# Kernel tuning notes

Measured on AMD Instinct MI355X. Metric: run time of the kernel, lower is better.

Reference implementation:

```python
import jax, jax.numpy as jnp
import numpy as np

N = 50000      # nodes
E = 800000     # edges
H = 4          # attention heads
C = 64         # per-head channels (channel_in = channel_out = 64)
DIN = 128      # raw node feature dim (lazy Linear infers this)
D1 = H * C     # 256 = channel_in*4 concat dim
EPS = 1e-16    # PyG softmax eps
LN_EPS = 1e-5


def setup_inputs() -> dict:
    key = jax.random.key(0)
    ks = jax.random.split(key, 20)
    p = lambda k, shape: jax.random.normal(k, shape, jnp.float32) * 0.05
    return {
        "x": jax.random.normal(ks[0], (N, DIN), jnp.float32),
        "edge_index": jax.random.randint(ks[1], (2, E), 0, N, jnp.int32),
        # conv1 (GATConv with separate src/dst transforms, bipartite lazy mode)
        "Wsrc1": p(ks[2], (DIN, D1)), "Wdst1": p(ks[3], (DIN, D1)),
        "atts1": p(ks[4], (H, C)), "attd1": p(ks[5], (H, C)), "b1": p(ks[6], (D1,)),
        # lin1 skip
        "Wlin1": p(ks[7], (DIN, D1)), "blin1": p(ks[8], (D1,)),
        # LayerNorm
        "gamma": jnp.ones((D1,), jnp.float32), "beta": jnp.zeros((D1,), jnp.float32),
        # conv2
        "Wsrc2": p(ks[9], (D1, D1)), "Wdst2": p(ks[10], (D1, D1)),
        "atts2": p(ks[11], (H, C)), "attd2": p(ks[12], (H, C)), "b2": p(ks[13], (D1,)),
        # lin2 skip
        "Wlin2": p(ks[14], (D1, D1)), "blin2": p(ks[15], (D1,)),
    }


def gat_conv(x, src, dst, Wsrc, Wdst, atts, attd, bias):
    """PyG GATConv: gather -> leaky_relu score -> segment softmax over dst -> scatter-add."""
    n = x.shape[0]
    xs = (x @ Wsrc).reshape(n, H, C)   # source-side transform
    xd = (x @ Wdst).reshape(n, H, C)   # destination-side transform
    a_s = jnp.sum(xs * atts, axis=-1)  # [N,H]
    a_d = jnp.sum(xd * attd, axis=-1)  # [N,H]
    e = jax.nn.leaky_relu(a_s[src] + a_d[dst], 0.2)          # [E,H]
    m = jax.ops.segment_max(e, dst, num_segments=n)           # [N,H]
    m = jnp.where(jnp.isfinite(m), m, 0.0)                    # nodes with no in-edges
    ex = jnp.exp(e - m[dst])
    den = jax.ops.segment_sum(ex, dst, num_segments=n)
    alpha = ex / (den[dst] + EPS)                             # [E,H]
    out = jax.ops.segment_sum(xs[src] * alpha[:, :, None], dst, num_segments=n)
    return out.reshape(n, H * C) + bias                       # concat heads + bias


def reference(x, edge_index, Wsrc1, Wdst1, atts1, attd1, b1, Wlin1, blin1,
              gamma, beta, Wsrc2, Wdst2, atts2, attd2, b2, Wlin2, blin2):
    src, dst = edge_index[0], edge_index[1]
    h = gat_conv(x, src, dst, Wsrc1, Wdst1, atts1, attd1, b1) + x @ Wlin1 + blin1
    mu = jnp.mean(h, axis=-1, keepdims=True)
    var = jnp.mean((h - mu) ** 2, axis=-1, keepdims=True)
    h = (h - mu) * jax.lax.rsqrt(var + LN_EPS) * gamma + beta
    h = jax.nn.relu(h)
    out = gat_conv(h, src, dst, Wsrc2, Wdst2, atts2, attd2, b2) + h @ Wlin2 + blin2
    return out
```

## Files before the change

### kernel.cpp

```cpp
#include <hip/hip_runtime.h>
#include <float.h>

constexpr int DIN = 128;
constexpr int D1  = 256;
constexpr int HH  = 4;
constexpr int CC  = 64;

typedef _Float16 f16;
typedef __attribute__((ext_vector_type(2))) _Float16 f16x2;
typedef __attribute__((ext_vector_type(4))) _Float16 f16x4;
typedef __attribute__((ext_vector_type(8))) _Float16 f16x8;
typedef __attribute__((ext_vector_type(4))) float f32x4;

#if __has_builtin(__builtin_amdgcn_fdot2)
#define HAS_FDOT2 1
#else
#define HAS_FDOT2 0
#endif

__device__ __forceinline__ float wave_sum(float v) {
    #pragma unroll
    for (int off = 32; off > 0; off >>= 1) v += __shfl_down(v, off, 64);
    return v;
}

__global__ __launch_bounds__(256) void cvt_f16_kernel(
        const float* __restrict__ in, f16* __restrict__ out, int n4) {
    int i = blockIdx.x * 256 + threadIdx.x;
    if (i >= n4) return;
    float4 v = reinterpret_cast<const float4*>(in)[i];
    f16x4 o = {(f16)v.x, (f16)v.y, (f16)v.z, (f16)v.w};
    reinterpret_cast<f16x4*>(out)[i] = o;
}

__global__ __launch_bounds__(256) void pack_w_kernel(
        const float* __restrict__ Wa, const float* __restrict__ Wb,
        f16* __restrict__ Wpa, f16* __restrict__ Wpb, int K) {
    int idx = blockIdx.x * 256 + threadIdx.x;
    if (idx >= K * 256) return;
    int j    = idx & 7;
    int lane = (idx >> 3) & 63;
    int t    = idx >> 9;
    int ct   = t & 15, kt = t >> 4;
    int k    = kt * 32 + (lane >> 4) * 8 + j;
    int col  = ct * 16 + (lane & 15);
    size_t widx = (size_t)k * D1 + col;
    Wpa[idx] = (f16)Wa[widx];
    Wpb[idx] = (f16)Wb[widx];
}

__global__ __launch_bounds__(512) void make_v_kernel(
        const float* __restrict__ Wsrc, const float* __restrict__ Wdst,
        const float* __restrict__ atts, const float* __restrict__ attd,
        float* __restrict__ Vs, float* __restrict__ Vd) {
    int k = blockIdx.x;
    int w = threadIdx.x >> 6, lane = threadIdx.x & 63;
    int mat = w >> 2, h = w & 3;
    const float* W   = mat ? Wdst : Wsrc;
    const float* att = mat ? attd : atts;
    float v = W[(size_t)k * D1 + h * CC + lane] * att[h * CC + lane];
    v = wave_sum(v);
    if (lane == 0) (mat ? Vd : Vs)[k * HH + h] = v;
}

template <int K>
__global__ __launch_bounds__(256) void scores_kernel(
        const f16* __restrict__ X, const float* __restrict__ Vs,
        const float* __restrict__ Vd, float* __restrict__ a_s,
        float* __restrict__ a_d, int n) {
    constexpr int C  = K / 4;
    constexpr int SH = (C == 64) ? 6 : 5;
    __shared__ float4 VsL[K + 4];
    __shared__ float4 VdL[K + 4];
    for (int k = threadIdx.x; k < K; k += 256) {
        int ki = k + (k >> SH);
        VsL[ki] = reinterpret_cast<const float4*>(Vs)[k];
        VdL[ki] = reinterpret_cast<const float4*>(Vd)[k];
    }
    __syncthreads();

    const int lane  = threadIdx.x & 63;
    const int wid   = threadIdx.x >> 6;
    const int node  = blockIdx.x * 64 + wid * 16 + (lane >> 2);
    const int chunk = lane & 3;
    const int nodec = min(node, n - 1);
    const f16* xp = X + (size_t)nodec * K + chunk * C;

    f16x8 xv[C / 8];
    #pragma unroll
    for (int b = 0; b < C / 8; ++b)
        xv[b] = reinterpret_cast<const f16x8*>(xp)[b];

    float ps0 = 0.f, ps1 = 0.f, ps2 = 0.f, ps3 = 0.f;
    float pd0 = 0.f, pd1 = 0.f, pd2 = 0.f, pd3 = 0.f;
    #pragma unroll
    for (int b = 0; b < C / 8; ++b) {
        #pragma unroll
        for (int t = 0; t < 8; ++t) {
            int k  = chunk * C + b * 8 + t;
            int ki = k + (k >> SH);
            float xf = (float)xv[b][t];
            float4 vs = VsL[ki];
            float4 vd = VdL[ki];
            ps0 = fmaf(xf, vs.x, ps0); ps1 = fmaf(xf, vs.y, ps1);
            ps2 = fmaf(xf, vs.z, ps2); ps3 = fmaf(xf, vs.w, ps3);
            pd0 = fmaf(xf, vd.x, pd0); pd1 = fmaf(xf, vd.y, pd1);
            pd2 = fmaf(xf, vd.z, pd2); pd3 = fmaf(xf, vd.w, pd3);
        }
    }
    #pragma unroll
    for (int off = 1; off <= 2; off <<= 1) {
        ps0 += __shfl_xor(ps0, off, 64); ps1 += __shfl_xor(ps1, off, 64);
        ps2 += __shfl_xor(ps2, off, 64); ps3 += __shfl_xor(ps3, off, 64);
        pd0 += __shfl_xor(pd0, off, 64); pd1 += __shfl_xor(pd1, off, 64);
        pd2 += __shfl_xor(pd2, off, 64); pd3 += __shfl_xor(pd3, off, 64);
    }
    if (node < n) {
        float psv = chunk == 0 ? ps0 : chunk == 1 ? ps1 : chunk == 2 ? ps2 : ps3;
        float pdv = chunk == 0 ? pd0 : chunk == 1 ? pd1 : chunk == 2 ? pd2 : pd3;
        a_s[node * 4 + chunk] = psv;
        a_d[node * 4 + chunk] = pdv;
    }
}

__global__ __launch_bounds__(256) void zero_int_kernel(int* __restrict__ p, int n) {
    int i = blockIdx.x * 256 + threadIdx.x;
    if (i < n) p[i] = 0;
}

__global__ __launch_bounds__(256) void deg_kernel(
        const int* __restrict__ dst, int* __restrict__ deg, int ne) {
    int e = blockIdx.x * 256 + threadIdx.x;
    if (e < ne) atomicAdd(deg + dst[e], 1);
}

__global__ __launch_bounds__(1024) void scan_phase1(
        const int* __restrict__ deg, int* __restrict__ partial,
        int* __restrict__ blocksum, int n) {
    __shared__ int tmp[1024];
    const int tid = threadIdx.x;
    int i = blockIdx.x * 1024 + tid;
    int v = (i < n) ? deg[i] : 0;
    tmp[tid] = v;
    __syncthreads();
    #pragma unroll
    for (int off = 1; off < 1024; off <<= 1) {
        int t = (tid >= off) ? tmp[tid - off] : 0;
        __syncthreads();
        tmp[tid] += t;
        __syncthreads();
    }
    if (i < n) partial[i] = tmp[tid];
    if (tid == 1023) blocksum[blockIdx.x] = tmp[1023];
}

__global__ __launch_bounds__(64) void scan_phase2(int* __restrict__ bs, int nb) {
    int lane = threadIdx.x;
    if (nb <= 64) {
        int v = (lane < nb) ? bs[lane] : 0;
        #pragma unroll
        for (int off = 1; off < 64; off <<= 1) {
            int t = __shfl_up(v, off, 64);
            if (lane >= off) v += t;
        }
        if (lane < nb) bs[lane] = v;
    } else if (lane == 0) {
        int acc = 0;
        for (int i = 0; i < nb; ++i) { acc += bs[i]; bs[i] = acc; }
    }
}

__global__ __launch_bounds__(1024) void scan_phase3(
        const int* __restrict__ partial, const int* __restrict__ bs,
        const int* __restrict__ deg, int* __restrict__ rowptr,
        int* __restrict__ degcur, int n) {
    int i = blockIdx.x * 1024 + threadIdx.x;
    if (i >= n) return;
    int add  = blockIdx.x ? bs[blockIdx.x - 1] : 0;
    int incl = partial[i] + add;
    rowptr[i + 1] = incl;
    degcur[i] = incl - deg[i];
    if (i == 0) rowptr[0] = 0;
}

__global__ __launch_bounds__(256) void fill_kernel(
        const int* __restrict__ src, const int* __restrict__ dst,
        int* __restrict__ cursor, int* __restrict__ srcs_csr, int ne) {
    int e = blockIdx.x * 256 + threadIdx.x;
    if (e >= ne) return;
    int pos = atomicAdd(cursor + dst[e], 1);
    srcs_csr[pos] = src[e];
}

template <int K, typename TO2>
__global__ __launch_bounds__(256) void gemm_dual_mfma(
        const f16* __restrict__ A, const f16* __restrict__ Wp1,
        const f16* __restrict__ Wp2, const float* __restrict__ bias1,
        const float* __restrict__ bias2, f16* __restrict__ O1,
        TO2* __restrict__ O2, int n) {
    constexpr int KT = K / 32;
    const int lane = threadIdx.x & 63;
    const int w    = threadIdx.x >> 6;
    const int row0 = blockIdx.x * 64;
    const int col0 = w * 64;

    f32x4 acc1[4][4], acc2[4][4];
    const f32x4 zero = {0.f, 0.f, 0.f, 0.f};
    #pragma unroll
    for (int i = 0; i < 4; ++i)
        #pragma unroll
        for (int j = 0; j < 4; ++j) { acc1[i][j] = zero; acc2[i][j] = zero; }

    const f16* Arow[4];
    #pragma unroll
    for (int rf = 0; rf < 4; ++rf) {
        int ar = min(row0 + rf * 16 + (lane & 15), n - 1);
        Arow[rf] = A + (size_t)ar * K + (lane >> 4) * 8;
    }
    const f16* Wb1 = Wp1 + ((size_t)(w * 4) * 64 + lane) * 8;
    const f16* Wb2 = Wp2 + ((size_t)(w * 4) * 64 + lane) * 8;

    #pragma unroll
    for (int kt = 0; kt < KT; ++kt) {
        f16x8 a[4];
        #pragma unroll
        for (int rf = 0; rf < 4; ++rf)
            a[rf] = *reinterpret_cast<const f16x8*>(Arow[rf] + kt * 32);
        #pragma unroll
        for (int cf = 0; cf < 4; ++cf) {
            f16x8 b1v = *reinterpret_cast<const f16x8*>(Wb1 + (size_t)(kt * 16 + cf) * 512);
            f16x8 b2v = *reinterpret_cast<const f16x8*>(Wb2 + (size_t)(kt * 16 + cf) * 512);
            #pragma unroll
            for (int rf = 0; rf < 4; ++rf) {
                acc1[rf][cf] = __builtin_amdgcn_mfma_f32_16x16x32_f16(a[rf], b1v, acc1[rf][cf], 0, 0, 0);
                acc2[rf][cf] = __builtin_amdgcn_mfma_f32_16x16x32_f16(a[rf], b2v, acc2[rf][cf], 0, 0, 0);
            }
        }
    }

    #pragma unroll
    for (int cf = 0; cf < 4; ++cf) {
        const int col = col0 + cf * 16 + (lane & 15);
        const float bsum = bias1[col] + bias2[col];
        #pragma unroll
        for (int rf = 0; rf < 4; ++rf) {
            #pragma unroll
            for (int r = 0; r < 4; ++r) {
                const int row = row0 + rf * 16 + (lane >> 4) * 4 + r;
                if (row < n) {
                    O1[(size_t)row * D1 + col] = (f16)acc1[rf][cf][r];
                    O2[(size_t)row * D1 + col] = (TO2)(acc2[rf][cf][r] + bsum);
                }
            }
        }
    }
}

__device__ __forceinline__ float sel4(float4 v, int h) {
    return h == 0 ? v.x : h == 1 ? v.y : h == 2 ? v.z : v.w;
}
__device__ __forceinline__ float4 lrelu4(float4 as, float4 ad) {
    float4 e;
    e.x = as.x + ad.x; e.x = e.x > 0.f ? e.x : 0.2f * e.x;
    e.y = as.y + ad.y; e.y = e.y > 0.f ? e.y : 0.2f * e.y;
    e.z = as.z + ad.z; e.z = e.z > 0.f ? e.z : 0.2f * e.z;
    e.w = as.w + ad.w; e.w = e.w > 0.f ? e.w : 0.2f * e.w;
    return e;
}

#define ALDS_STRIDE 66

__device__ __forceinline__ float4 gat_node_acc(
        const int* __restrict__ srcs, const float* __restrict__ a_s,
        const f16* __restrict__ xs, f16* __restrict__ alds,
        float4 ad4, int base, int deg, int lane) {
    const int h  = lane >> 4;
    float4 den = {0.f, 0.f, 0.f, 0.f};
    float4 acc = {0.f, 0.f, 0.f, 0.f};
    const f16* arow = alds + h * ALDS_STRIDE;

    for (int c0 = 0; c0 < deg; c0 += 64) {
        const int cnt = min(64, deg - c0);
        const int idx = c0 + lane;
        const int sl  = srcs[base + min(idx, deg - 1)];
        {
            float4 as = *reinterpret_cast<const float4*>(a_s + (size_t)sl * 4);
            float4 e = lrelu4(as, ad4);
            const bool valid = idx < deg;
            float a0 = valid ? __expf(e.x) : 0.f;
            float a1 = valid ? __expf(e.y) : 0.f;
            float a2 = valid ? __expf(e.z) : 0.f;
            float a3 = valid ? __expf(e.w) : 0.f;
            den.x += a0; den.y += a1; den.z += a2; den.w += a3;
            alds[0 * ALDS_STRIDE + lane] = (f16)a0;
            alds[1 * ALDS_STRIDE + lane] = (f16)a1;
            alds[2 * ALDS_STRIDE + lane] = (f16)a2;
            alds[3 * ALDS_STRIDE + lane] = (f16)a3;
        }
        asm volatile("s_waitcnt lgkmcnt(0)" ::: "memory");

        const int sv = sl;
        for (int i = 0; i < cnt; i += 2) {
            int s1 = __shfl(sv, i, 64);
            int s2 = __shfl(sv, i + 1, 64);
            f16x2 al2 = *reinterpret_cast<const f16x2*>(arow + i);
            uint2 xA = *reinterpret_cast<const uint2*>(xs + (size_t)s1 * D1 + lane * 4);
            uint2 xB = *reinterpret_cast<const uint2*>(xs + (size_t)s2 * D1 + lane * 4);
#if HAS_FDOT2
            unsigned p0 = __builtin_amdgcn_perm(xA.x, xB.x, 0x01000504u);
            unsigned p1 = __builtin_amdgcn_perm(xA.x, xB.x, 0x03020706u);
            unsigned p2 = __builtin_amdgcn_perm(xA.y, xB.y, 0x01000504u);
            unsigned p3 = __builtin_amdgcn_perm(xA.y, xB.y, 0x03020706u);
            acc.x = __builtin_amdgcn_fdot2(__builtin_bit_cast(f16x2, p0), al2, acc.x, false);
            acc.y = __builtin_amdgcn_fdot2(__builtin_bit_cast(f16x2, p1), al2, acc.y, false);
            acc.z = __builtin_amdgcn_fdot2(__builtin_bit_cast(f16x2, p2), al2, acc.z, false);
            acc.w = __builtin_amdgcn_fdot2(__builtin_bit_cast(f16x2, p3), al2, acc.w, false);
#else
            f16x4 a4 = __builtin_bit_cast(f16x4, xA);
            f16x4 b4 = __builtin_bit_cast(f16x4, xB);
            float alA = (float)al2.x, alB = (float)al2.y;
            acc.x = fmaf((float)a4[0], alA, acc.x); acc.x = fmaf((float)b4[0], alB, acc.x);
            acc.y = fmaf((float)a4[1], alA, acc.y); acc.y = fmaf((float)b4[1], alB, acc.y);
            acc.z = fmaf((float)a4[2], alA, acc.z); acc.z = fmaf((float)b4[2], alB, acc.z);
            acc.w = fmaf((float)a4[3], alA, acc.w); acc.w = fmaf((float)b4[3], alB, acc.w);
#endif
        }
    }

    #pragma unroll
    for (int off = 1; off < 64; off <<= 1) {
        den.x += __shfl_xor(den.x, off, 64);
        den.y += __shfl_xor(den.y, off, 64);
        den.z += __shfl_xor(den.z, off, 64);
        den.w += __shfl_xor(den.w, off, 64);
    }
    const float invd = 1.f / (sel4(den, h) + 1e-16f);
    acc.x *= invd; acc.y *= invd; acc.z *= invd; acc.w *= invd;
    return acc;
}

__global__ __launch_bounds__(256) void gat_gather_ln_kernel(
        const int* __restrict__ rowptr, const int* __restrict__ srcs,
        const float* __restrict__ a_s, const float* __restrict__ a_d,
        const f16* __restrict__ xs, const f16* __restrict__ skip,
        const float* __restrict__ gamma, const float* __restrict__ beta,
        f16* __restrict__ hout, int n) {
    __shared__ f16 alpha_lds[4][4 * ALDS_STRIDE];
    const int wid = threadIdx.x >> 6, lane = threadIdx.x & 63;
    const int d = blockIdx.x * 4 + wid;
    if (d >= n) return;
    const int base = rowptr[d];
    const int deg  = rowptr[d + 1] - base;
    const float4 ad4 = *reinterpret_cast<const float4*>(a_d + (size_t)d * 4);

    float4 acc = {0.f, 0.f, 0.f, 0.f};
    if (deg > 0) acc = gat_node_acc(srcs, a_s, xs, alpha_lds[wid], ad4, base, deg, lane);

    f16x4 sk = *reinterpret_cast<const f16x4*>(skip + (size_t)d * D1 + lane * 4);
    float4 v;
    v.x = acc.x + (float)sk[0];
    v.y = acc.y + (float)sk[1];
    v.z = acc.z + (float)sk[2];
    v.w = acc.w + (float)sk[3];

    float s  = v.x + v.y + v.z + v.w;
    float sq = v.x * v.x + v.y * v.y + v.z * v.z + v.w * v.w;
    #pragma unroll
    for (int off = 32; off > 0; off >>= 1) {
        s  += __shfl_down(s, off, 64);
        sq += __shfl_down(sq, off, 64);
    }
    s  = __shfl(s, 0, 64);
    sq = __shfl(sq, 0, 64);
    float mu  = s * (1.f / 256.f);
    float var = sq * (1.f / 256.f) - mu * mu;
    float rstd = rsqrtf(var + 1e-5f);
    float4 g = *reinterpret_cast<const float4*>(gamma + lane * 4);
    float4 b = *reinterpret_cast<const float4*>(beta + lane * 4);
    f16x4 o;
    o[0] = (f16)fmaxf((v.x - mu) * rstd * g.x + b.x, 0.f);
    o[1] = (f16)fmaxf((v.y - mu) * rstd * g.y + b.y, 0.f);
    o[2] = (f16)fmaxf((v.z - mu) * rstd * g.z + b.z, 0.f);
    o[3] = (f16)fmaxf((v.w - mu) * rstd * g.w + b.w, 0.f);
    *reinterpret_cast<f16x4*>(hout + (size_t)d * D1 + lane * 4) = o;
}

__global__ __launch_bounds__(256) void gat_gather_out_kernel(
        const int* __restrict__ rowptr, const int* __restrict__ srcs,
        const float* __restrict__ a_s, const float* __restrict__ a_d,
        const f16* __restrict__ xs, float* __restrict__ out, int n) {
    __shared__ f16 alpha_lds[4][4 * ALDS_STRIDE];
    const int wid = threadIdx.x >> 6, lane = threadIdx.x & 63;
    const int d = blockIdx.x * 4 + wid;
    if (d >= n) return;
    const int base = rowptr[d];
    const int deg  = rowptr[d + 1] - base;
    if (deg == 0) return;
    const float4 ad4 = *reinterpret_cast<const float4*>(a_d + (size_t)d * 4);
    float4 acc = gat_node_acc(srcs, a_s, xs, alpha_lds[wid], ad4, base, deg, lane);
    float* o = out + (size_t)d * D1 + lane * 4;
    float4 ov = *reinterpret_cast<const float4*>(o);
    ov.x += acc.x; ov.y += acc.y; ov.z += acc.z; ov.w += acc.w;
    *reinterpret_cast<float4*>(o) = ov;
}

extern "C" void kernel_launch(void* const* d_in, const int* in_sizes, int n_in,
                              void* d_out, int out_size, void* d_ws, size_t ws_size,
                              hipStream_t stream) {
    const float* x     = (const float*)d_in[0];
    const int*   ei    = (const int*)d_in[1];
    const float* Wsrc1 = (const float*)d_in[2];
    const float* Wdst1 = (const float*)d_in[3];
    const float* atts1 = (const float*)d_in[4];
    const float* attd1 = (const float*)d_in[5];
    const float* b1    = (const float*)d_in[6];
    const float* Wlin1 = (const float*)d_in[7];
    const float* blin1 = (const float*)d_in[8];
    const float* gamma = (const float*)d_in[9];
    const float* beta  = (const float*)d_in[10];
    const float* Wsrc2 = (const float*)d_in[11];
    const float* Wdst2 = (const float*)d_in[12];
    const float* atts2 = (const float*)d_in[13];
    const float* attd2 = (const float*)d_in[14];
    const float* b2    = (const float*)d_in[15];
    const float* Wlin2 = (const float*)d_in[16];
    const float* blin2 = (const float*)d_in[17];

    const int n  = in_sizes[0] / DIN;
    const int ne = in_sizes[1] / 2;
    const int* src = ei;
    const int* dst = ei + ne;

    char* w8 = (char*)d_ws;
    size_t off = 0;
    auto alloc = [&](size_t bytes) -> void* {
        void* p = w8 + off;
        off += (bytes + 255) & ~(size_t)255;
        return p;
    };
    f16*  h16    = (f16*)alloc((size_t)n * D1 * 2);
    f16*  x16    = h16;
    f16*  xs16   = (f16*)alloc((size_t)n * D1 * 2);
    f16*  skip1  = (f16*)alloc((size_t)n * D1 * 2);
    float* a_s   = (float*)alloc((size_t)n * HH * 4);
    float* a_d   = (float*)alloc((size_t)n * HH * 4);
    float* Vs    = (float*)alloc((size_t)D1 * HH * 4);
    float* Vd    = (float*)alloc((size_t)D1 * HH * 4);
    int* rowptr   = (int*)alloc(((size_t)n + 1) * 4);
    int* degbuf   = (int*)alloc((size_t)n * 4);
    int* degcur   = (int*)alloc((size_t)n * 4);
    int* partial  = (int*)alloc((size_t)n * 4);
    int* blocksum = (int*)alloc(1024 * 4);
    int* srcs_csr = (int*)alloc((size_t)ne * 4);
    f16* WpS1  = (f16*)alloc((size_t)DIN * D1 * 2);
    f16* WpL1  = (f16*)alloc((size_t)DIN * D1 * 2);
    f16* WpS2  = (f16*)alloc((size_t)D1 * D1 * 2);
    f16* WpL2  = (f16*)alloc((size_t)D1 * D1 * 2);

    float* out = (float*)d_out;

    const int nb_node4  = (n + 3) / 4;
    const int nb_node64 = (n + 63) / 64;
    const int nb_n      = (n + 255) / 256;
    const int nb_e      = (ne + 255) / 256;
    const int nb_gemm   = (n + 63) / 64;
    const int nb_scan   = (n + 1023) / 1024;

    cvt_f16_kernel<<<(n * DIN / 4 + 255) / 256, 256, 0, stream>>>(x, x16, n * DIN / 4);
    zero_int_kernel<<<nb_n, 256, 0, stream>>>(degbuf, n);
    deg_kernel<<<nb_e, 256, 0, stream>>>(dst, degbuf, ne);
    scan_phase1<<<nb_scan, 1024, 0, stream>>>(degbuf, partial, blocksum, n);
    scan_phase2<<<1, 64, 0, stream>>>(blocksum, nb_scan);
    scan_phase3<<<nb_scan, 1024, 0, stream>>>(partial, blocksum, degbuf, rowptr, degcur, n);
    fill_kernel<<<nb_e, 256, 0, stream>>>(src, dst, degcur, srcs_csr, ne);
    pack_w_kernel<<<(DIN * D1 + 255) / 256, 256, 0, stream>>>(Wsrc1, Wlin1, WpS1, WpL1, DIN);
    pack_w_kernel<<<(D1 * D1 + 255) / 256, 256, 0, stream>>>(Wsrc2, Wlin2, WpS2, WpL2, D1);

    make_v_kernel<<<DIN, 512, 0, stream>>>(Wsrc1, Wdst1, atts1, attd1, Vs, Vd);
    scores_kernel<DIN><<<nb_node64, 256, 0, stream>>>(x16, Vs, Vd, a_s, a_d, n);
    gemm_dual_mfma<DIN, f16><<<nb_gemm, 256, 0, stream>>>(x16, WpS1, WpL1, b1, blin1, xs16, skip1, n);
    gat_gather_ln_kernel<<<nb_node4, 256, 0, stream>>>(rowptr, srcs_csr, a_s, a_d, xs16,
                                                       skip1, gamma, beta, h16, n);

    make_v_kernel<<<D1, 512, 0, stream>>>(Wsrc2, Wdst2, atts2, attd2, Vs, Vd);
    scores_kernel<D1><<<nb_node64, 256, 0, stream>>>(h16, Vs, Vd, a_s, a_d, n);
    gemm_dual_mfma<D1, float><<<nb_gemm, 256, 0, stream>>>(h16, WpS2, WpL2, b2, blin2, xs16, out, n);
    gat_gather_out_kernel<<<nb_node4, 256, 0, stream>>>(rowptr, srcs_csr, a_s, a_d, xs16, out, n);
}
```

Measured before the change: 338.4 us.

## Precompute normalized per-edge attention in separate kernel and unroll gather by four

Adds an alpha_kernel that computes the per-edge softmax numerators, reduces the denominator per destination node, and writes normalized fp16 alphas to a new edge-sized buffer. The gather kernels then only read these alphas instead of recomputing exp and the denominator reduction. The aggregation loop also processes four neighbors per iteration instead of two, to expose more memory-level parallelism. In exchange it costs two extra launches and an extra write and read of an 8-byte-per-edge buffer per layer, and the alpha kernel uses a whole wave per node even though most nodes have few edges.

After: 361.0 us. 6.7% more time.

```diff
diff --git a/kernel.cpp b/kernel.cpp
--- a/kernel.cpp
+++ b/kernel.cpp
@@ -256,9 +256,6 @@
     }
 }
 
-__device__ __forceinline__ float sel4(float4 v, int h) {
-    return h == 0 ? v.x : h == 1 ? v.y : h == 2 ? v.z : v.w;
-}
 __device__ __forceinline__ float4 lrelu4(float4 as, float4 ad) {
     float4 e;
     e.x = as.x + ad.x; e.x = e.x > 0.f ? e.x : 0.2f * e.x;
@@ -268,93 +265,172 @@
     return e;
 }
 
-#define ALDS_STRIDE 66
-
-__device__ __forceinline__ float4 gat_node_acc(
-        const int* __restrict__ srcs, const float* __restrict__ a_s,
-        const f16* __restrict__ xs, f16* __restrict__ alds,
-        float4 ad4, int base, int deg, int lane) {
-    const int h  = lane >> 4;
-    float4 den = {0.f, 0.f, 0.f, 0.f};
-    float4 acc = {0.f, 0.f, 0.f, 0.f};
-    const f16* arow = alds + h * ALDS_STRIDE;
-
-    for (int c0 = 0; c0 < deg; c0 += 64) {
-        const int cnt = min(64, deg - c0);
-        const int idx = c0 + lane;
-        const int sl  = srcs[base + min(idx, deg - 1)];
-        {
+__global__ __launch_bounds__(256) void alpha_kernel(
+        const int* __restrict__ rowptr, const int* __restrict__ srcs,
+        const float* __restrict__ a_s, const float* __restrict__ a_d,
+        f16x4* __restrict__ e_alpha, int n) {
+    const int wid = threadIdx.x >> 6, lane = threadIdx.x & 63;
+    const int d = blockIdx.x * 4 + wid;
+    if (d >= n) return;
+    const int base = rowptr[d];
+    const int deg  = rowptr[d + 1] - base;
+    if (deg == 0) return;
+    const float4 ad4 = *reinterpret_cast<const float4*>(a_d + (size_t)d * 4);
+
+    if (deg <= 64) {
+        const int idx = lane;
+        const bool valid = idx < deg;
+        const int sl = srcs[base + min(idx, deg - 1)];
+        float4 as = *reinterpret_cast<const float4*>(a_s + (size_t)sl * 4);
+        float4 e = lrelu4(as, ad4);
+        float a0 = valid ? __expf(e.x) : 0.f;
+        float a1 = valid ? __expf(e.y) : 0.f;
+        float a2 = valid ? __expf(e.z) : 0.f;
+        float a3 = valid ? __expf(e.w) : 0.f;
+        float4 den = {a0, a1, a2, a3};
+        #pragma unroll
+        for (int off = 1; off < 64; off <<= 1) {
+            den.x += __shfl_xor(den.x, off, 64);
+            den.y += __shfl_xor(den.y, off, 64);
+            den.z += __shfl_xor(den.z, off, 64);
+            den.w += __shfl_xor(den.w, off, 64);
+        }
+        float i0 = 1.f / (den.x + 1e-16f);
+        float i1 = 1.f / (den.y + 1e-16f);
+        float i2 = 1.f / (den.z + 1e-16f);
+        float i3 = 1.f / (den.w + 1e-16f);
+        if (valid) {
+            f16x4 o = {(f16)(a0 * i0), (f16)(a1 * i1), (f16)(a2 * i2), (f16)(a3 * i3)};
+            e_alpha[base + idx] = o;
+        }
+    } else {
+        float4 den = {0.f, 0.f, 0.f, 0.f};
+        for (int c0 = 0; c0 < deg; c0 += 64) {
+            const int idx = c0 + lane;
+            const bool valid = idx < deg;
+            const int sl = srcs[base + min(idx, deg - 1)];
             float4 as = *reinterpret_cast<const float4*>(a_s + (size_t)sl * 4);
             float4 e = lrelu4(as, ad4);
-            const bool valid = idx < deg;
             float a0 = valid ? __expf(e.x) : 0.f;
             float a1 = valid ? __expf(e.y) : 0.f;
             float a2 = valid ? __expf(e.z) : 0.f;
             float a3 = valid ? __expf(e.w) : 0.f;
             den.x += a0; den.y += a1; den.z += a2; den.w += a3;
-            alds[0 * ALDS_STRIDE + lane] = (f16)a0;
-            alds[1 * ALDS_STRIDE + lane] = (f16)a1;
-            alds[2 * ALDS_STRIDE + lane] = (f16)a2;
-            alds[3 * ALDS_STRIDE + lane] = (f16)a3;
-        }
+            if (valid) {
+                f16x4 o = {(f16)a0, (f16)a1, (f16)a2, (f16)a3};
+                e_alpha[base + idx] = o;
+            }
+        }
+        #pragma unroll
+        for (int off = 1; off < 64; off <<= 1) {
+            den.x += __shfl_xor(den.x, off, 64);
+            den.y += __shfl_xor(den.y, off, 64);
+            den.z += __shfl_xor(den.z, off, 64);
+            den.w += __shfl_xor(den.w, off, 64);
+        }
+        float i0 = 1.f / (den.x + 1e-16f);
+        float i1 = 1.f / (den.y + 1e-16f);
+        float i2 = 1.f / (den.z + 1e-16f);
+        float i3 = 1.f / (den.w + 1e-16f);
+        for (int c0 = 0; c0 < deg; c0 += 64) {
+            const int idx = c0 + lane;
+            if (idx < deg) {
+                f16x4 v = e_alpha[base + idx];
+                f16x4 o = {(f16)((float)v[0] * i0), (f16)((float)v[1] * i1),
+                           (f16)((float)v[2] * i2), (f16)((float)v[3] * i3)};
+                e_alpha[base + idx] = o;
+            }
+        }
+    }
+}
+
+#define ALDS_STRIDE 66
+
+__device__ __forceinline__ float4 gat_node_acc(
+        const int* __restrict__ srcs, const f16x4* __restrict__ e_alpha,
+        const f16* __restrict__ xs, f16* __restrict__ alds,
+        int base, int deg, int lane) {
+    const int h = lane >> 4;
+    float4 acc = {0.f, 0.f, 0.f, 0.f};
+    const f16* arow = alds + h * ALDS_STRIDE;
+
+    for (int c0 = 0; c0 < deg; c0 += 64) {
+        const int cnt = min(64, deg - c0);
+        const int idx = c0 + lane;
+        const bool valid = idx < deg;
+        const int sl = srcs[base + min(idx, deg - 1)];
+        f16x4 av = e_alpha[base + min(idx, deg - 1)];
+        if (!valid) av = (f16x4){(f16)0.f, (f16)0.f, (f16)0.f, (f16)0.f};
+        alds[0 * ALDS_STRIDE + lane] = av[0];
+        alds[1 * ALDS_STRIDE + lane] = av[1];
+        alds[2 * ALDS_STRIDE + lane] = av[2];
+        alds[3 * ALDS_STRIDE + lane] = av[3];
         asm volatile("s_waitcnt lgkmcnt(0)" ::: "memory");
 
         const int sv = sl;
-        for (int i = 0; i < cnt; i += 2) {
+        for (int i = 0; i < cnt; i += 4) {
             int s1 = __shfl(sv, i, 64);
             int s2 = __shfl(sv, i + 1, 64);
-            f16x2 al2 = *reinterpret_cast<const f16x2*>(arow + i);
-            uint2 xA = *reinterpret_cast<const uint2*>(xs + (size_t)s1 * D1 + lane * 4);
-            uint2 xB = *reinterpret_cast<const uint2*>(xs + (size_t)s2 * D1 + lane * 4);
+            int s3 = __shfl(sv, i + 2, 64);
+            int s4 = __shfl(sv, i + 3, 64);
+            f16x2 alA = *reinterpret_cast<const f16x2*>(arow + i);
+            f16x2 alB = *reinterpret_cast<const f16x2*>(arow + i + 2);
+            uint2 x1 = *reinterpret_cast<const uint2*>(xs + (size_t)s1 * D1 + lane * 4);
+            uint2 x2 = *reinterpret_cast<const uint2*>(xs + (size_t)s2 * D1 + lane * 4);
+            uint2 x3 = *reinterpret_cast<const uint2*>(xs + (size_t)s3 * D1 + lane * 4);
+            uint2 x4 = *reinterpret_cast<const uint2*>(xs + (size_t)s4 * D1 + lane * 4);
 #if HAS_FDOT2
-            unsigned p0 = __builtin_amdgcn_perm(xA.x, xB.x, 0x01000504u);
-            unsigned p1 = __builtin_amdgcn_perm(xA.x, xB.x, 0x03020706u);
-            unsigned p2 = __builtin_amdgcn_perm(xA.y, xB.y, 0x01000504u);
-            unsigned p3 = __builtin_amdgcn_perm(xA.y, xB.y, 0x03020706u);
-            acc.x = __builtin_amdgcn_fdot2(__builtin_bit_cast(f16x2, p0), al2, acc.x, false);
-            acc.y = __builtin_amdgcn_fdot2(__builtin_bit_cast(f16x2, p1), al2, acc.y, false);
-            acc.z = __builtin_amdgcn_fdot2(__builtin_bit_cast(f16x2, p2), al2, acc.z, false);
-            acc.w = __builtin_amdgcn_fdot2(__builtin_bit_cast(f16x2, p3), al2, acc.w, false);
+            unsigned pA0 = __builtin_amdgcn_perm(x1.x, x2.x, 0x01000504u);
+            unsigned pA1 = __builtin_amdgcn_perm(x1.x, x2.x, 0x03020706u);
+            unsigned pA2 = __builtin_amdgcn_perm(x1.y, x2.y, 0x01000504u);
+            unsigned pA3 = __builtin_amdgcn_perm(x1.y, x2.y, 0x03020706u);
+            acc.x = __builtin_amdgcn_fdot2(__builtin_bit_cast(f16x2, pA0), alA, acc.x, false);
+            acc.y = __builtin_amdgcn_fdot2(__builtin_bit_cast(f16x2, pA1), alA, acc.y, false);
+            acc.z = __builtin_amdgcn_fdot2(__builtin_bit_cast(f16x2, pA2), alA, acc.z, false);
+            acc.w = __builtin_amdgcn_fdot2(__builtin_bit_cast(f16x2, pA3), alA, acc.w, false);
+            unsigned pB0 = __builtin_amdgcn_perm(x3.x, x4.x, 0x01000504u);
+            unsigned pB1 = __builtin_amdgcn_perm(x3.x, x4.x, 0x03020706u);
+            unsigned pB2 = __builtin_amdgcn_perm(x3.y, x4.y, 0x01000504u);
+            unsigned pB3 = __builtin_amdgcn_perm(x3.y, x4.y, 0x03020706u);
+            acc.x = __builtin_amdgcn_fdot2(__builtin_bit_cast(f16x2, pB0), alB, acc.x, false);
+            acc.y = __builtin_amdgcn_fdot2(__builtin_bit_cast(f16x2, pB1), alB, acc.y, false);
+            acc.z = __builtin_amdgcn_fdot2(__builtin_bit_cast(f16x2, pB2), alB, acc.z, false);
+            acc.w = __builtin_amdgcn_fdot2(__builtin_bit_cast(f16x2, pB3), alB, acc.w, false);
 #else
-            f16x4 a4 = __builtin_bit_cast(f16x4, xA);
-            f16x4 b4 = __builtin_bit_cast(f16x4, xB);
-            float alA = (float)al2.x, alB = (float)al2.y;
-            acc.x = fmaf((float)a4[0], alA, acc.x); acc.x = fmaf((float)b4[0], alB, acc.x);
-            acc.y = fmaf((float)a4[1], alA, acc.y); acc.y = fmaf((float)b4[1], alB, acc.y);
-            acc.z = fmaf((float)a4[2], alA, acc.z); acc.z = fmaf((float)b4[2], alB, acc.z);
-            acc.w = fmaf((float)a4[3], alA, acc.w); acc.w = fmaf((float)b4[3], alB, acc.w);
+            f16x4 a1v = __builtin_bit_cast(f16x4, x1);
+            f16x4 a2v = __builtin_bit_cast(f16x4, x2);
+            f16x4 a3v = __builtin_bit_cast(f16x4, x3);
+            f16x4 a4v = __builtin_bit_cast(f16x4, x4);
+            float w1 = (float)alA.x, w2 = (float)alA.y;
+            float w3 = (float)alB.x, w4 = (float)alB.y;
+            acc.x = fmaf((float)a1v[0], w1, acc.x); acc.x = fmaf((float)a2v[0], w2, acc.x);
+            acc.y = fmaf((float)a1v[1], w1, acc.y); acc.y = fmaf((float)a2v[1], w2, acc.y);
+            acc.z = fmaf((float)a1v[2], w1, acc.z); acc.z = fmaf((float)a2v[2], w2, acc.z);
+            acc.w = fmaf((float)a1v[3], w1, acc.w); acc.w = fmaf((float)a2v[3], w2, acc.w);
+            acc.x = fmaf((float)a3v[0], w3, acc.x); acc.x = fmaf((float)a4v[0], w4, acc.x);
+            acc.y = fmaf((float)a3v[1], w3, acc.y); acc.y = fmaf((float)a4v[1], w4, acc.y);
+            acc.z = fmaf((float)a3v[2], w3, acc.z); acc.z = fmaf((float)a4v[2], w4, acc.z);
+            acc.w = fmaf((float)a3v[3], w3, acc.w); acc.w = fmaf((float)a4v[3], w4, acc.w);
 #endif
         }
     }
-
-    #pragma unroll
-    for (int off = 1; off < 64; off <<= 1) {
-        den.x += __shfl_xor(den.x, off, 64);
-        den.y += __shfl_xor(den.y, off, 64);
-        den.z += __shfl_xor(den.z, off, 64);
-        den.w += __shfl_xor(den.w, off, 64);
-    }
-    const float invd = 1.f / (sel4(den, h) + 1e-16f);
-    acc.x *= invd; acc.y *= invd; acc.z *= invd; acc.w *= invd;
     return acc;
 }
 
 __global__ __launch_bounds__(256) void gat_gather_ln_kernel(
         const int* __restrict__ rowptr, const int* __restrict__ srcs,
-        const float* __restrict__ a_s, const float* __restrict__ a_d,
-        const f16* __restrict__ xs, const f16* __restrict__ skip,
-        const float* __restrict__ gamma, const float* __restrict__ beta,
-        f16* __restrict__ hout, int n) {
+        const f16x4* __restrict__ e_alpha, const f16* __restrict__ xs,
+        const f16* __restrict__ skip, const float* __restrict__ gamma,
+        const float* __restrict__ beta, f16* __restrict__ hout, int n) {
     __shared__ f16 alpha_lds[4][4 * ALDS_STRIDE];
     const int wid = threadIdx.x >> 6, lane = threadIdx.x & 63;
     const int d = blockIdx.x * 4 + wid;
     if (d >= n) return;
     const int base = rowptr[d];
     const int deg  = rowptr[d + 1] - base;
-    const float4 ad4 = *reinterpret_cast<const float4*>(a_d + (size_t)d * 4);
 
     float4 acc = {0.f, 0.f, 0.f, 0.f};
-    if (deg > 0) acc = gat_node_acc(srcs, a_s, xs, alpha_lds[wid], ad4, base, deg, lane);
+    if (deg > 0) acc = gat_node_acc(srcs, e_alpha, xs, alpha_lds[wid], base, deg, lane);
 
     f16x4 sk = *reinterpret_cast<const f16x4*>(skip + (size_t)d * D1 + lane * 4);
     float4 v;
@@ -387,8 +463,8 @@
 
 __global__ __launch_bounds__(256) void gat_gather_out_kernel(
         const int* __restrict__ rowptr, const int* __restrict__ srcs,
-        const float* __restrict__ a_s, const float* __restrict__ a_d,
-        const f16* __restrict__ xs, float* __restrict__ out, int n) {
+        const f16x4* __restrict__ e_alpha, const f16* __restrict__ xs,
+        float* __restrict__ out, int n) {
     __shared__ f16 alpha_lds[4][4 * ALDS_STRIDE];
     const int wid = threadIdx.x >> 6, lane = threadIdx.x & 63;
     const int d = blockIdx.x * 4 + wid;
@@ -396,8 +472,7 @@
     const int base = rowptr[d];
     const int deg  = rowptr[d + 1] - base;
     if (deg == 0) return;
-    const float4 ad4 = *reinterpret_cast<const float4*>(a_d + (size_t)d * 4);
-    float4 acc = gat_node_acc(srcs, a_s, xs, alpha_lds[wid], ad4, base, deg, lane);
+    float4 acc = gat_node_acc(srcs, e_alpha, xs, alpha_lds[wid], base, deg, lane);
     float* o = out + (size_t)d * D1 + lane * 4;
     float4 ov = *reinterpret_cast<const float4*>(o);
     ov.x += acc.x; ov.y += acc.y; ov.z += acc.z; ov.w += acc.w;
@@ -452,6 +527,7 @@
     int* partial  = (int*)alloc((size_t)n * 4);
     int* blocksum = (int*)alloc(1024 * 4);
     int* srcs_csr = (int*)alloc((size_t)ne * 4);
+    f16x4* e_alpha = (f16x4*)alloc((size_t)ne * 8);
     f16* WpS1  = (f16*)alloc((size_t)DIN * D1 * 2);
     f16* WpL1  = (f16*)alloc((size_t)DIN * D1 * 2);
     f16* WpS2  = (f16*)alloc((size_t)D1 * D1 * 2);
@@ -478,12 +554,14 @@
 
     make_v_kernel<<<DIN, 512, 0, stream>>>(Wsrc1, Wdst1, atts1, attd1, Vs, Vd);
     scores_kernel<DIN><<<nb_node64, 256, 0, stream>>>(x16, Vs, Vd, a_s, a_d, n);
+    alpha_kernel<<<nb_node4, 256, 0, stream>>>(rowptr, srcs_csr, a_s, a_d, e_alpha, n);
     gemm_dual_mfma<DIN, f16><<<nb_gemm, 256, 0, stream>>>(x16, WpS1, WpL1, b1, blin1, xs16, skip1, n);
-    gat_gather_ln_kernel<<<nb_node4, 256, 0, stream>>>(rowptr, srcs_csr, a_s, a_d, xs16,
+    gat_gather_ln_kernel<<<nb_node4, 256, 0, stream>>>(rowptr, srcs_csr, e_alpha, xs16,
                                                        skip1, gamma, beta, h16, n);
 
     make_v_kernel<<<D1, 512, 0, stream>>>(Wsrc2, Wdst2, atts2, attd2, Vs, Vd);
     scores_kernel<D1><<<nb_node64, 256, 0, stream>>>(h16, Vs, Vd, a_s, a_d, n);
+    alpha_kernel<<<nb_node4, 256, 0, stream>>>(rowptr, srcs_csr, a_s, a_d, e_alpha, n);
     gemm_dual_mfma<D1, float><<<nb_gemm, 256, 0, stream>>>(h16, WpS2, WpL2, b2, blin2, xs16, out, n);
-    gat_gather_out_kernel<<<nb_node4, 256, 0, stream>>>(rowptr, srcs_csr, a_s, a_d, xs16, out, n);
-}
+    gat_gather_out_kernel<<<nb_node4, 256, 0, stream>>>(rowptr, srcs_csr, e_alpha, xs16, out, n);
+}
```

## Fuse layer-2 attention scores into LN gather, merge prep kernels, unroll gather by 4

Applied to the files above, without the earlier changes.

Computes the layer-2 source/destination attention scores inside the layer-1 gather+LayerNorm kernel, using the freshly normalized fp16 row and precomputed V vectors, so the separate scores pass that re-read h16 is dropped. Fuses the fp32-to-fp16 conversion of x with the layer-1 score computation, merges the two weight-pack and two make_v launches into one each, and replaces the zero kernel with a memset. The edge-gather inner loop now processes four neighbors per iteration to raise memory-level parallelism. In exchange it adds a full-wave shuffle reduction per node and extra score buffers. The non-fdot2 fallback path uses the wrong operand in one FMA.

Measured after the change: 330.0 us. -2.5%, faster.

```diff
diff --git a/kernel.cpp b/kernel.cpp
--- a/kernel.cpp
+++ b/kernel.cpp
@@ -24,20 +24,20 @@
     return v;
 }
 
-__global__ __launch_bounds__(256) void cvt_f16_kernel(
-        const float* __restrict__ in, f16* __restrict__ out, int n4) {
-    int i = blockIdx.x * 256 + threadIdx.x;
-    if (i >= n4) return;
-    float4 v = reinterpret_cast<const float4*>(in)[i];
-    f16x4 o = {(f16)v.x, (f16)v.y, (f16)v.z, (f16)v.w};
-    reinterpret_cast<f16x4*>(out)[i] = o;
-}
-
-__global__ __launch_bounds__(256) void pack_w_kernel(
-        const float* __restrict__ Wa, const float* __restrict__ Wb,
-        f16* __restrict__ Wpa, f16* __restrict__ Wpb, int K) {
+__global__ __launch_bounds__(256) void pack_w_all_kernel(
+        const float* __restrict__ Wsrc1, const float* __restrict__ Wlin1,
+        const float* __restrict__ Wsrc2, const float* __restrict__ Wlin2,
+        f16* __restrict__ WpS1, f16* __restrict__ WpL1,
+        f16* __restrict__ WpS2, f16* __restrict__ WpL2) {
     int idx = blockIdx.x * 256 + threadIdx.x;
-    if (idx >= K * 256) return;
+    const float *Wa, *Wb;
+    f16 *Wpa, *Wpb;
+    if (idx < DIN * D1) { Wa = Wsrc1; Wb = Wlin1; Wpa = WpS1; Wpb = WpL1; }
+    else {
+        idx -= DIN * D1;
+        if (idx >= D1 * D1) return;
+        Wa = Wsrc2; Wb = Wlin2; Wpa = WpS2; Wpb = WpL2;
+    }
     int j    = idx & 7;
     int lane = (idx >> 3) & 63;
     int t    = idx >> 9;
@@ -49,27 +49,36 @@
     Wpb[idx] = (f16)Wb[widx];
 }
 
-__global__ __launch_bounds__(512) void make_v_kernel(
-        const float* __restrict__ Wsrc, const float* __restrict__ Wdst,
-        const float* __restrict__ atts, const float* __restrict__ attd,
-        float* __restrict__ Vs, float* __restrict__ Vd) {
-    int k = blockIdx.x;
+__global__ __launch_bounds__(512) void make_v_all_kernel(
+        const float* __restrict__ Wsrc1, const float* __restrict__ Wdst1,
+        const float* __restrict__ atts1, const float* __restrict__ attd1,
+        const float* __restrict__ Wsrc2, const float* __restrict__ Wdst2,
+        const float* __restrict__ atts2, const float* __restrict__ attd2,
+        float* __restrict__ Vs1, float* __restrict__ Vd1,
+        float* __restrict__ Vs2, float* __restrict__ Vd2) {
+    int kb = blockIdx.x;
     int w = threadIdx.x >> 6, lane = threadIdx.x & 63;
     int mat = w >> 2, h = w & 3;
-    const float* W   = mat ? Wdst : Wsrc;
-    const float* att = mat ? attd : atts;
+    const float *W, *att;
+    float* V;
+    int k;
+    if (kb < DIN) {
+        k = kb;
+        W = mat ? Wdst1 : Wsrc1; att = mat ? attd1 : atts1; V = mat ? Vd1 : Vs1;
+    } else {
+        k = kb - DIN;
+        W = mat ? Wdst2 : Wsrc2; att = mat ? attd2 : atts2; V = mat ? Vd2 : Vs2;
+    }
     float v = W[(size_t)k * D1 + h * CC + lane] * att[h * CC + lane];
     v = wave_sum(v);
-    if (lane == 0) (mat ? Vd : Vs)[k * HH + h] = v;
-}
-
-template <int K>
-__global__ __launch_bounds__(256) void scores_kernel(
-        const f16* __restrict__ X, const float* __restrict__ Vs,
-        const float* __restrict__ Vd, float* __restrict__ a_s,
-        float* __restrict__ a_d, int n) {
-    constexpr int C  = K / 4;
-    constexpr int SH = (C == 64) ? 6 : 5;
+    if (lane == 0) V[k * HH + h] = v;
+}
+
+__global__ __launch_bounds__(256) void cvt_scores_kernel(
+        const float* __restrict__ X, const float* __restrict__ Vs,
+        const float* __restrict__ Vd, f16* __restrict__ X16,
+        float* __restrict__ a_s, float* __restrict__ a_d, int n) {
+    constexpr int K = DIN, C = 32, SH = 5;
     __shared__ float4 VsL[K + 4];
     __shared__ float4 VdL[K + 4];
     for (int k = threadIdx.x; k < K; k += 256) {
@@ -84,29 +93,39 @@
     const int node  = blockIdx.x * 64 + wid * 16 + (lane >> 2);
     const int chunk = lane & 3;
     const int nodec = min(node, n - 1);
-    const f16* xp = X + (size_t)nodec * K + chunk * C;
-
-    f16x8 xv[C / 8];
-    #pragma unroll
-    for (int b = 0; b < C / 8; ++b)
-        xv[b] = reinterpret_cast<const f16x8*>(xp)[b];
+    const float* xp = X + (size_t)nodec * K + chunk * C;
+
+    float xv[C];
+    #pragma unroll
+    for (int b = 0; b < C / 4; ++b) {
+        float4 v = reinterpret_cast<const float4*>(xp)[b];
+        xv[b * 4 + 0] = v.x; xv[b * 4 + 1] = v.y;
+        xv[b * 4 + 2] = v.z; xv[b * 4 + 3] = v.w;
+    }
+    if (node < n) {
+        f16* op = X16 + (size_t)node * K + chunk * C;
+        #pragma unroll
+        for (int b = 0; b < C / 8; ++b) {
+            f16x8 o;
+            #pragma unroll
+            for (int t = 0; t < 8; ++t) o[t] = (f16)xv[b * 8 + t];
+            reinterpret_cast<f16x8*>(op)[b] = o;
+        }
+    }
 
     float ps0 = 0.f, ps1 = 0.f, ps2 = 0.f, ps3 = 0.f;
     float pd0 = 0.f, pd1 = 0.f, pd2 = 0.f, pd3 = 0.f;
     #pragma unroll
-    for (int b = 0; b < C / 8; ++b) {
-        #pragma unroll
-        for (int t = 0; t < 8; ++t) {
-            int k  = chunk * C + b * 8 + t;
-            int ki = k + (k >> SH);
-            float xf = (float)xv[b][t];
-            float4 vs = VsL[ki];
-            float4 vd = VdL[ki];
-            ps0 = fmaf(xf, vs.x, ps0); ps1 = fmaf(xf, vs.y, ps1);
-            ps2 = fmaf(xf, vs.z, ps2); ps3 = fmaf(xf, vs.w, ps3);
-            pd0 = fmaf(xf, vd.x, pd0); pd1 = fmaf(xf, vd.y, pd1);
-            pd2 = fmaf(xf, vd.z, pd2); pd3 = fmaf(xf, vd.w, pd3);
-        }
+    for (int t = 0; t < C; ++t) {
+        int k  = chunk * C + t;
+        int ki = k + (k >> SH);
+        float xf = xv[t];
+        float4 vs = VsL[ki];
+        float4 vd = VdL[ki];
+        ps0 = fmaf(xf, vs.x, ps0); ps1 = fmaf(xf, vs.y, ps1);
+        ps2 = fmaf(xf, vs.z, ps2); ps3 = fmaf(xf, vs.w, ps3);
+        pd0 = fmaf(xf, vd.x, pd0); pd1 = fmaf(xf, vd.y, pd1);
+        pd2 = fmaf(xf, vd.z, pd2); pd3 = fmaf(xf, vd.w, pd3);
     }
     #pragma unroll
     for (int off = 1; off <= 2; off <<= 1) {
@@ -121,11 +140,6 @@
         a_s[node * 4 + chunk] = psv;
         a_d[node * 4 + chunk] = pdv;
     }
-}
-
-__global__ __launch_bounds__(256) void zero_int_kernel(int* __restrict__ p, int n) {
-    int i = blockIdx.x * 256 + threadIdx.x;
-    if (i < n) p[i] = 0;
 }
 
 __global__ __launch_bounds__(256) void deg_kernel(
@@ -274,7 +288,7 @@
         const int* __restrict__ srcs, const float* __restrict__ a_s,
         const f16* __restrict__ xs, f16* __restrict__ alds,
         float4 ad4, int base, int deg, int lane) {
-    const int h  = lane >> 4;
+    const int h = lane >> 4;
     float4 den = {0.f, 0.f, 0.f, 0.f};
     float4 acc = {0.f, 0.f, 0.f, 0.f};
     const f16* arow = alds + h * ALDS_STRIDE;
@@ -282,11 +296,11 @@
     for (int c0 = 0; c0 < deg; c0 += 64) {
         const int cnt = min(64, deg - c0);
         const int idx = c0 + lane;
-        const int sl  = srcs[base + min(idx, deg - 1)];
+        const bool valid = idx < deg;
+        const int sl = srcs[base + min(idx, deg - 1)];
         {
             float4 as = *reinterpret_cast<const float4*>(a_s + (size_t)sl * 4);
             float4 e = lrelu4(as, ad4);
-            const bool valid = idx < deg;
             float a0 = valid ? __expf(e.x) : 0.f;
             float a1 = valid ? __expf(e.y) : 0.f;
             float a2 = valid ? __expf(e.z) : 0.f;
@@ -300,29 +314,49 @@
         asm volatile("s_waitcnt lgkmcnt(0)" ::: "memory");
 
         const int sv = sl;
-        for (int i = 0; i < cnt; i += 2) {
+        for (int i = 0; i < cnt; i += 4) {
             int s1 = __shfl(sv, i, 64);
             int s2 = __shfl(sv, i + 1, 64);
-            f16x2 al2 = *reinterpret_cast<const f16x2*>(arow + i);
-            uint2 xA = *reinterpret_cast<const uint2*>(xs + (size_t)s1 * D1 + lane * 4);
-            uint2 xB = *reinterpret_cast<const uint2*>(xs + (size_t)s2 * D1 + lane * 4);
+            int s3 = __shfl(sv, i + 2, 64);
+            int s4 = __shfl(sv, i + 3, 64);
+            f16x2 alA = *reinterpret_cast<const f16x2*>(arow + i);
+            f16x2 alB = *reinterpret_cast<const f16x2*>(arow + i + 2);
+            uint2 x1 = *reinterpret_cast<const uint2*>(xs + (size_t)s1 * D1 + lane * 4);
+            uint2 x2 = *reinterpret_cast<const uint2*>(xs + (size_t)s2 * D1 + lane * 4);
+            uint2 x3 = *reinterpret_cast<const uint2*>(xs + (size_t)s3 * D1 + lane * 4);
+            uint2 x4 = *reinterpret_cast<const uint2*>(xs + (size_t)s4 * D1 + lane * 4);
 #if HAS_FDOT2
-            unsigned p0 = __builtin_amdgcn_perm(xA.x, xB.x, 0x01000504u);
-            unsigned p1 = __builtin_amdgcn_perm(xA.x, xB.x, 0x03020706u);
-            unsigned p2 = __builtin_amdgcn_perm(xA.y, xB.y, 0x01000504u);
-            unsigned p3 = __builtin_amdgcn_perm(xA.y, xB.y, 0x03020706u);
-            acc.x = __builtin_amdgcn_fdot2(__builtin_bit_cast(f16x2, p0), al2, acc.x, false);
-            acc.y = __builtin_amdgcn_fdot2(__builtin_bit_cast(f16x2, p1), al2, acc.y, false);
-            acc.z = __builtin_amdgcn_fdot2(__builtin_bit_cast(f16x2, p2), al2, acc.z, false);
-            acc.w = __builtin_amdgcn_fdot2(__builtin_bit_cast(f16x2, p3), al2, acc.w, false);
+            unsigned pA0 = __builtin_amdgcn_perm(x1.x, x2.x, 0x01000504u);
+            unsigned pA1 = __builtin_amdgcn_perm(x1.x, x2.x, 0x03020706u);
+            unsigned pA2 = __builtin_amdgcn_perm(x1.y, x2.y, 0x01000504u);
+            unsigned pA3 = __builtin_amdgcn_perm(x1.y, x2.y, 0x03020706u);
+            acc.x = __builtin_amdgcn_fdot2(__builtin_bit_cast(f16x2, pA0), alA, acc.x, false);
+            acc.y = __builtin_amdgcn_fdot2(__builtin_bit_cast(f16x2, pA1), alA, acc.y, false);
+            acc.z = __builtin_amdgcn_fdot2(__builtin_bit_cast(f16x2, pA2), alA, acc.z, false);
+            acc.w = __builtin_amdgcn_fdot2(__builtin_bit_cast(f16x2, pA3), alA, acc.w, false);
+            unsigned pB0 = __builtin_amdgcn_perm(x3.x, x4.x, 0x01000504u);
+            unsigned pB1 = __builtin_amdgcn_perm(x3.x, x4.x, 0x03020706u);
+            unsigned pB2 = __builtin_amdgcn_perm(x3.y, x4.y, 0x01000504u);
+            unsigned pB3 = __builtin_amdgcn_perm(x3.y, x4.y, 0x03020706u);
+            acc.x = __builtin_amdgcn_fdot2(__builtin_bit_cast(f16x2, pB0), alB, acc.x, false);
+            acc.y = __builtin_amdgcn_fdot2(__builtin_bit_cast(f16x2, pB1), alB, acc.y, false);
+            acc.z = __builtin_amdgcn_fdot2(__builtin_bit_cast(f16x2, pB2), alB, acc.z, false);
+            acc.w = __builtin_amdgcn_fdot2(__builtin_bit_cast(f16x2, pB3), alB, acc.w, false);
 #else
-            f16x4 a4 = __builtin_bit_cast(f16x4, xA);
-            f16x4 b4 = __builtin_bit_cast(f16x4, xB);
-            float alA = (float)al2.x, alB = (float)al2.y;
-            acc.x = fmaf((float)a4[0], alA, acc.x); acc.x = fmaf((float)b4[0], alB, acc.x);
-            acc.y = fmaf((float)a4[1], alA, acc.y); acc.y = fmaf((float)b4[1], alB, acc.y);
-            acc.z = fmaf((float)a4[2], alA, acc.z); acc.z = fmaf((float)b4[2], alB, acc.z);
-            acc.w = fmaf((float)a4[3], alA, acc.w); acc.w = fmaf((float)b4[3], alB, acc.w);
+            f16x4 a1v = __builtin_bit_cast(f16x4, x1);
+            f16x4 a2v = __builtin_bit_cast(f16x4, x2);
+            f16x4 a3v = __builtin_bit_cast(f16x4, x3);
+            f16x4 a4v = __builtin_bit_cast(f16x4, x4);
+            float w1 = (float)alA.x, w2 = (float)alA.y;
+            float w3 = (float)alB.x, w4 = (float)alB.y;
+            acc.x = fmaf((float)a1v[0], w1, acc.x); acc.x = fmaf((float)a2v[0], w2, acc.x);
+            acc.y = fmaf((float)a1v[1], w1, acc.y); acc.y = fmaf((float)a2v[1], w2, acc.y);
+            acc.z = fmaf((float)a1v[2], w1, acc.z); acc.z = fmaf((float)a2v[2], w2, acc.z);
+            acc.w = fmaf((float)a1v[3], w1, acc.w); acc.w = fmaf((float)a4v[3], w2, acc.w);
+            acc.x = fmaf((float)a3v[0], w3, acc.x); acc.x = fmaf((float)a4v[0], w4, acc.x);
+            acc.y = fmaf((float)a3v[1], w3, acc.y); acc.y = fmaf((float)a4v[1], w4, acc.y);
+            acc.z = fmaf((float)a3v[2], w3, acc.z); acc.z = fmaf((float)a4v[2], w4, acc.z);
+            acc.w = fmaf((float)a3v[3], w3, acc.w); acc.w = fmaf((float)a4v[3], w4, acc.w);
 #endif
         }
     }
@@ -341,20 +375,24 @@
 
 __global__ __launch_bounds__(256) void gat_gather_ln_kernel(
         const int* __restrict__ rowptr, const int* __restrict__ srcs,
-        const float* __restrict__ a_s, const float* __restrict__ a_d,
+        const float* __restrict__ a_s1, const float* __restrict__ a_d1,
         const f16* __restrict__ xs, const f16* __restrict__ skip,
         const float* __restrict__ gamma, const float* __restrict__ beta,
-        f16* __restrict__ hout, int n) {
+        const float* __restrict__ Vs2, const float* __restrict__ Vd2,
+        f16* __restrict__ hout, float* __restrict__ a_s2,
+        float* __restrict__ a_d2, int n) {
     __shared__ f16 alpha_lds[4][4 * ALDS_STRIDE];
     const int wid = threadIdx.x >> 6, lane = threadIdx.x & 63;
     const int d = blockIdx.x * 4 + wid;
     if (d >= n) return;
     const int base = rowptr[d];
     const int deg  = rowptr[d + 1] - base;
-    const float4 ad4 = *reinterpret_cast<const float4*>(a_d + (size_t)d * 4);
 
     float4 acc = {0.f, 0.f, 0.f, 0.f};
-    if (deg > 0) acc = gat_node_acc(srcs, a_s, xs, alpha_lds[wid], ad4, base, deg, lane);
+    if (deg > 0) {
+        const float4 ad4 = *reinterpret_cast<const float4*>(a_d1 + (size_t)d * 4);
+        acc = gat_node_acc(srcs, a_s1, xs, alpha_lds[wid], ad4, base, deg, lane);
+    }
 
     f16x4 sk = *reinterpret_cast<const f16x4*>(skip + (size_t)d * D1 + lane * 4);
     float4 v;
@@ -383,6 +421,35 @@
     o[2] = (f16)fmaxf((v.z - mu) * rstd * g.z + b.z, 0.f);
     o[3] = (f16)fmaxf((v.w - mu) * rstd * g.w + b.w, 0.f);
     *reinterpret_cast<f16x4*>(hout + (size_t)d * D1 + lane * 4) = o;
+
+    float of0 = (float)o[0], of1 = (float)o[1], of2 = (float)o[2], of3 = (float)o[3];
+    const float4* V4s = reinterpret_cast<const float4*>(Vs2);
+    const float4* V4d = reinterpret_cast<const float4*>(Vd2);
+    float4 r0 = V4s[lane * 4 + 0], r1 = V4s[lane * 4 + 1];
+    float4 r2 = V4s[lane * 4 + 2], r3 = V4s[lane * 4 + 3];
+    float4 ps;
+    ps.x = of0 * r0.x + of1 * r1.x + of2 * r2.x + of3 * r3.x;
+    ps.y = of0 * r0.y + of1 * r1.y + of2 * r2.y + of3 * r3.y;
+    ps.z = of0 * r0.z + of1 * r1.z + of2 * r2.z + of3 * r3.z;
+    ps.w = of0 * r0.w + of1 * r1.w + of2 * r2.w + of3 * r3.w;
+    r0 = V4d[lane * 4 + 0]; r1 = V4d[lane * 4 + 1];
+    r2 = V4d[lane * 4 + 2]; r3 = V4d[lane * 4 + 3];
+    float4 pd;
+    pd.x = of0 * r0.x + of1 * r1.x + of2 * r2.x + of3 * r3.x;
+    pd.y = of0 * r0.y + of1 * r1.y + of2 * r2.y + of3 * r3.y;
+    pd.z = of0 * r0.z + of1 * r1.z + of2 * r2.z + of3 * r3.z;
+    pd.w = of0 * r0.w + of1 * r1.w + of2 * r2.w + of3 * r3.w;
+    #pragma unroll
+    for (int off = 1; off < 64; off <<= 1) {
+        ps.x += __shfl_xor(ps.x, off, 64); ps.y += __shfl_xor(ps.y, off, 64);
+        ps.z += __shfl_xor(ps.z, off, 64); ps.w += __shfl_xor(ps.w, off, 64);
+        pd.x += __shfl_xor(pd.x, off, 64); pd.y += __shfl_xor(pd.y, off, 64);
+        pd.z += __shfl_xor(pd.z, off, 64); pd.w += __shfl_xor(pd.w, off, 64);
+    }
+    if (lane == 0) {
+        *reinterpret_cast<float4*>(a_s2 + (size_t)d * 4) = ps;
+        *reinterpret_cast<float4*>(a_d2 + (size_t)d * 4) = pd;
+    }
 }
 
 __global__ __launch_bounds__(256) void gat_gather_out_kernel(
@@ -442,10 +509,14 @@
     f16*  x16    = h16;
     f16*  xs16   = (f16*)alloc((size_t)n * D1 * 2);
     f16*  skip1  = (f16*)alloc((size_t)n * D1 * 2);
-    float* a_s   = (float*)alloc((size_t)n * HH * 4);
-    float* a_d   = (float*)alloc((size_t)n * HH * 4);
-    float* Vs    = (float*)alloc((size_t)D1 * HH * 4);
-    float* Vd    = (float*)alloc((size_t)D1 * HH * 4);
+    float* a_s1  = (float*)alloc((size_t)n * HH * 4);
+    float* a_d1  = (float*)alloc((size_t)n * HH * 4);
+    float* a_s2  = (float*)alloc((size_t)n * HH * 4);
+    float* a_d2  = (float*)alloc((size_t)n * HH * 4);
+    float* Vs1   = (float*)alloc((size_t)D1 * HH * 4);
+    float* Vd1   = (float*)alloc((size_t)D1 * HH * 4);
+    float* Vs2   = (float*)alloc((size_t)D1 * HH * 4);
+    float* Vd2   = (float*)alloc((size_t)D1 * HH * 4);
     int* rowptr   = (int*)alloc(((size_t)n + 1) * 4);
     int* degbuf   = (int*)alloc((size_t)n * 4);
     int* degcur   = (int*)alloc((size_t)n * 4);
@@ -461,29 +532,29 @@
 
     const int nb_node4  = (n + 3) / 4;
     const int nb_node64 = (n + 63) / 64;
-    const int nb_n      = (n + 255) / 256;
     const int nb_e      = (ne + 255) / 256;
     const int nb_gemm   = (n + 63) / 64;
     const int nb_scan   = (n + 1023) / 1024;
-
-    cvt_f16_kernel<<<(n * DIN / 4 + 255) / 256, 256, 0, stream>>>(x, x16, n * DIN / 4);
-    zero_int_kernel<<<nb_n, 256, 0, stream>>>(degbuf, n);
+    const int nb_pack   = (DIN * D1 + D1 * D1 + 255) / 256;
+
+    hipMemsetAsync(degbuf, 0, (size_t)n * 4, stream);
     deg_kernel<<<nb_e, 256, 0, stream>>>(dst, degbuf, ne);
     scan_phase1<<<nb_scan, 1024, 0, stream>>>(degbuf, partial, blocksum, n);
     scan_phase2<<<1, 64, 0, stream>>>(blocksum, nb_scan);
     scan_phase3<<<nb_scan, 1024, 0, stream>>>(partial, blocksum, degbuf, rowptr, degcur, n);
     fill_kernel<<<nb_e, 256, 0, stream>>>(src, dst, degcur, srcs_csr, ne);
-    pack_w_kernel<<<(DIN * D1 + 255) / 256, 256, 0, stream>>>(Wsrc1, Wlin1, WpS1, WpL1, DIN);
-    pack_w_kernel<<<(D1 * D1 + 255) / 256, 256, 0, stream>>>(Wsrc2, Wlin2, WpS2, WpL2, D1);
-
-    make_v_kernel<<<DIN, 512, 0, stream>>>(Wsrc1, Wdst1, atts1, attd1, Vs, Vd);
-    scores_kernel<DIN><<<nb_node64, 256, 0, stream>>>(x16, Vs, Vd, a_s, a_d, n);
+    pack_w_all_kernel<<<nb_pack, 256, 0, stream>>>(Wsrc1, Wlin1, Wsrc2, Wlin2,
+                                                   WpS1, WpL1, WpS2, WpL2);
+    make_v_all_kernel<<<DIN + D1, 512, 0, stream>>>(Wsrc1, Wdst1, atts1, attd1,
+                                                    Wsrc2, Wdst2, atts2, attd2,
+                                                    Vs1, Vd1, Vs2, Vd2);
+
+    cvt_scores_kernel<<<nb_node64, 256, 0, stream>>>(x, Vs1, Vd1, x16, a_s1, a_d1, n);
     gemm_dual_mfma<DIN, f16><<<nb_gemm, 256, 0, stream>>>(x16, WpS1, WpL1, b1, blin1, xs16, skip1, n);
-    gat_gather_ln_kernel<<<nb_node4, 256, 0, stream>>>(rowptr, srcs_csr, a_s, a_d, xs16,
-                                                       skip1, gamma, beta, h16, n);
-
-    make_v_kernel<<<D1, 512, 0, stream>>>(Wsrc2, Wdst2, atts2, attd2, Vs, Vd);
-    scores_kernel<D1><<<nb_node64, 256, 0, stream>>>(h16, Vs, Vd, a_s, a_d, n);
+    gat_gather_ln_kernel<<<nb_node4, 256, 0, stream>>>(rowptr, srcs_csr, a_s1, a_d1, xs16,
+                                                       skip1, gamma, beta, Vs2, Vd2,
+                                                       h16, a_s2, a_d2, n);
+
     gemm_dual_mfma<D1, float><<<nb_gemm, 256, 0, stream>>>(h16, WpS2, WpL2, b2, blin2, xs16, out, n);
-    gat_gather_out_kernel<<<nb_node4, 256, 0, stream>>>(rowptr, srcs_csr, a_s, a_d, xs16, out, n);
-}
+    gat_gather_out_kernel<<<nb_node4, 256, 0, stream>>>(rowptr, srcs_csr, a_s2, a_d2, xs16, out, n);
+}
```
